# Performance work log

Hardware: AMD Instinct MI355X
Metric: run time of the kernel (lower is better)

## Reference

```python
import jax, jax.numpy as jnp
import numpy as np

K_NEIGHBORS = 32  # n_neighbors, eval mode -> displacement = 0


def setup_inputs() -> dict:
    key = jax.random.key(0)
    ks = jax.random.split(key, 9)
    B, N, F = 1024, 200000, 64
    C, H = 16, 128
    return {
        "x": jax.random.normal(ks[0], (B, F), jnp.float32),
        "X_data": jax.random.normal(ks[1], (N, F), jnp.float32),
        "y": jax.random.uniform(ks[2], (N,), jnp.float32),
        "W_gate": jax.random.normal(ks[3], (F + 1, C), jnp.float32) / np.sqrt(F + 1),
        "b_gate": jax.random.normal(ks[4], (C,), jnp.float32) * 0.01,
        "W1": jax.random.normal(ks[5], (C + F, H), jnp.float32) / np.sqrt(C + F),
        "b1": jax.random.normal(ks[6], (H,), jnp.float32) * 0.01,
        "W_last": jax.random.normal(ks[7], (H, 1), jnp.float32) / np.sqrt(H),
        "b_last": jax.random.normal(ks[8], (1,), jnp.float32) * 0.01,
    }


def reference(x, X_data, y, W_gate, b_gate, W1, b1, W_last, b_last):
    # Euclidean (p=2) cdist via the expanded form: ||a-b||^2 = ||a||^2 + ||b||^2 - 2 a.b
    d2 = (jnp.sum(x * x, axis=1, keepdims=True)
          + jnp.sum(X_data * X_data, axis=1)[None, :]
          - 2.0 * (x @ X_data.T))                      # [B, N]
    dist = jnp.sqrt(jnp.maximum(d2, 0.0))
    # torch.argsort(distances,1)[:, :k] == indices of k smallest distances
    _, idx = jax.lax.top_k(-dist, K_NEIGHBORS)          # [B, K]
    neighbors = X_data[idx]                             # [B, K, F] gather
    neighbors_y = y[idx][..., None]                     # [B, K, 1]
    nf = jnp.concatenate([neighbors, neighbors_y], axis=2)  # [B, K, F+1]
    gated = jnp.tanh(nf @ W_gate + b_gate)              # [B, K, C]
    agg = jnp.sum(gated, axis=1)                        # [B, C]
    o = jnp.concatenate([x, agg], axis=1)               # [B, F+C]
    o = jnp.tanh(o @ W1 + b1)                           # activation_function = tanh
    o = jax.nn.sigmoid(o @ W_last + b_last)             # [B, 1]
    return o
```

## Files before the change

### kernel.cpp

```cpp
#include <hip/hip_runtime.h>
#include <cstdint>

#define FDIM 64
#define KNN 32
#define NBUCKET 256
#define MAXCAP 2048
#define SEG 8
#define OCAP 512
#define BANDQ 96

typedef unsigned int u32;
typedef unsigned long long u64;
typedef __attribute__((ext_vector_type(8))) short bf16x8;
typedef __attribute__((ext_vector_type(4))) float f32x4;

__device__ __forceinline__ void gload_lds16(const void* g, void* l) {
    __builtin_amdgcn_global_load_lds(
        (const __attribute__((address_space(1))) unsigned int*)g,
        (__attribute__((address_space(3))) unsigned int*)l,
        16, 0, 0);
}

__device__ __forceinline__ float load_query(const float* __restrict__ x, int q, float4* xv) {
    const float4* xp = (const float4*)(x + (size_t)q * FDIM);
    float n0 = 0.f, n1 = 0.f, n2 = 0.f, n3 = 0.f;
#pragma unroll
    for (int k = 0; k < 16; ++k) {
        float4 v = xp[k];
        xv[k] = v;
        n0 = fmaf(v.x, v.x, n0); n1 = fmaf(v.y, v.y, n1);
        n2 = fmaf(v.z, v.z, n2); n3 = fmaf(v.w, v.w, n3);
    }
    return (n0 + n1) + (n2 + n3);
}

__device__ __forceinline__ float dot_row(const float4* __restrict__ xv, const float* __restrict__ row) {
    const float4* rv = (const float4*)row;
    float d0 = 0.f, d1 = 0.f, d2 = 0.f, d3 = 0.f;
#pragma unroll
    for (int k = 0; k < 16; ++k) {
        float4 r = rv[k];
        float4 a = xv[k];
        d0 = fmaf(a.x, r.x, d0); d1 = fmaf(a.y, r.y, d1);
        d2 = fmaf(a.z, r.z, d2); d3 = fmaf(a.w, r.w, d3);
    }
    return (d0 + d1) + (d2 + d3);
}

__global__ __launch_bounds__(256) void k_xnorm(const float* __restrict__ X, float* __restrict__ Xn, int N) {
    int i = blockIdx.x * 256 + threadIdx.x;
    if (i >= N) return;
    const float4* r = (const float4*)(X + (size_t)i * FDIM);
    float d0 = 0.f, d1 = 0.f, d2 = 0.f, d3 = 0.f;
#pragma unroll
    for (int k = 0; k < 16; ++k) {
        float4 v = r[k];
        d0 = fmaf(v.x, v.x, d0); d1 = fmaf(v.y, v.y, d1);
        d2 = fmaf(v.z, v.z, d2); d3 = fmaf(v.w, v.w, d3);
    }
    Xn[i] = (d0 + d1) + (d2 + d3);
}

__global__ __launch_bounds__(256) void k_cvtT(const float* __restrict__ src, uint4* __restrict__ dst, int n_u4) {
    int i = blockIdx.x * 256 + threadIdx.x;
    if (i >= n_u4) return;
    int lane = i & 63;
    int kk = (i >> 6) & 1;
    int g = i >> 7;
    int row = g * 16 + (lane & 15);
    int col = kk * 32 + (lane >> 4) * 8;
    const float4* s = (const float4*)(src + (size_t)row * FDIM + col);
    float4 a = s[0], b = s[1];
    ushort o[8];
    const float* f = &a.x;
#pragma unroll
    for (int k = 0; k < 4; ++k) {
        u32 u = __float_as_uint(f[k]);
        o[k] = (ushort)((u + 0x7fffu + ((u >> 16) & 1u)) >> 16);
    }
    const float* gg = &b.x;
#pragma unroll
    for (int k = 0; k < 4; ++k) {
        u32 u = __float_as_uint(gg[k]);
        o[4 + k] = (ushort)((u + 0x7fffu + ((u >> 16) & 1u)) >> 16);
    }
    dst[i] = *(uint4*)o;
}

__global__ __launch_bounds__(256) void k_cvtT_norm(const float* __restrict__ src, uint4* __restrict__ dst,
                                                   float* __restrict__ norms, int n_u4) {
    __shared__ float pn[4][16];
    int t = threadIdx.x;
    int i = blockIdx.x * 256 + t;
    int lane = t & 63;
    int w = t >> 6;
    int kk = (i >> 6) & 1;
    int g = i >> 7;
    int r = lane & 15;
    int row = g * 16 + r;
    int col = kk * 32 + (lane >> 4) * 8;
    const float4* s = (const float4*)(src + (size_t)row * FDIM + col);
    float4 a = s[0], b = s[1];
    float n0 = fmaf(a.x, a.x, a.y * a.y);
    float n1 = fmaf(a.z, a.z, a.w * a.w);
    float n2 = fmaf(b.x, b.x, b.y * b.y);
    float n3 = fmaf(b.z, b.z, b.w * b.w);
    float ss = (n0 + n1) + (n2 + n3);
    ushort o[8];
    const float* f = &a.x;
#pragma unroll
    for (int k = 0; k < 4; ++k) {
        u32 u = __float_as_uint(f[k]);
        o[k] = (ushort)((u + 0x7fffu + ((u >> 16) & 1u)) >> 16);
    }
    const float* gg = &b.x;
#pragma unroll
    for (int k = 0; k < 4; ++k) {
        u32 u = __float_as_uint(gg[k]);
        o[4 + k] = (ushort)((u + 0x7fffu + ((u >> 16) & 1u)) >> 16);
    }
    dst[i] = *(uint4*)o;
    ss += __shfl_xor(ss, 16);
    ss += __shfl_xor(ss, 32);
    if (lane < 16) pn[w][r] = ss;
    __syncthreads();
    if (t < 32) {
        float v = (t < 16) ? (pn[0][t] + pn[1][t]) : (pn[2][t - 16] + pn[3][t - 16]);
        norms[blockIdx.x * 32 + t] = v;
    }
}

__global__ __launch_bounds__(256) void k_hist(const float* __restrict__ x, const float* __restrict__ X,
                                              const float* __restrict__ Xn, u32* __restrict__ hist,
                                              int N, int nsamp, int sj) {
    __shared__ unsigned char h8[NBUCKET * 256];
    int t = threadIdx.x;
    u32* h32 = (u32*)h8;
#pragma unroll
    for (int k = 0; k < 64; ++k) h32[k * 256 + t] = 0;
    __syncthreads();
    int q = blockIdx.x * 256 + t;
    float4 xv[16];
    float xn = load_query(x, q, xv);
    for (int j = 0; j < sj; ++j) {
        int s = blockIdx.y * sj + j;
        int p = s * 16;
        if (s < nsamp && p < N) {
            float dp = dot_row(xv, X + (size_t)p * FDIM);
            float d2 = fmaxf(xn + Xn[p] - 2.f * dp, 0.f);
            int b = min(NBUCKET - 1, (int)d2);
            int idx = b * 256 + t;
            unsigned char v = h8[idx];
            h8[idx] = (v == 255u) ? v : (unsigned char)(v + 1);
        }
    }
    __syncthreads();
#pragma unroll
    for (int w = 0; w < 128; ++w) {
        u32 v0 = h8[(2 * w) * 256 + t];
        u32 v1 = h8[(2 * w + 1) * 256 + t];
        if (v0 | v1) atomicAdd(&hist[(size_t)q * 128 + w], v0 | (v1 << 16));
    }
}

__global__ __launch_bounds__(256) void k_thresh(const u32* __restrict__ hist, float* __restrict__ Tq, int B) {
    int q = blockIdx.x * 256 + threadIdx.x;
    if (q >= B) return;
    const u32* h = hist + (size_t)q * 128;
    int cum = 0;
    float T = (float)NBUCKET;
    for (int w = 0; w < 128; ++w) {
        u32 v = h[w];
        cum += (int)(v & 0xffffu);
        if (cum >= KNN) { T = (float)(2 * w + 1); break; }
        cum += (int)(v >> 16);
        if (cum >= KNN) { T = (float)(2 * w + 2); break; }
    }
    Tq[q] = T + 2.0f;
}

__global__ __launch_bounds__(256, 3) void k_sample_d2(
        const uint4* __restrict__ xT, const uint4* __restrict__ XT,
        const float* __restrict__ qn, const float* __restrict__ Xn,
        unsigned char* __restrict__ d2s, int S) {
    int t = threadIdx.x;
    int w = t >> 6, lane = t & 63;
    int G = lane >> 4, r = lane & 15;
    int qg = blockIdx.x;
    int wq = qg * 128 + w * 32;
    int pb = blockIdx.y * 128;
    int Bq = gridDim.x * 128;

    bf16x8 afr[2][2];
#pragma unroll
    for (int kk = 0; kk < 2; ++kk)
#pragma unroll
        for (int mi = 0; mi < 2; ++mi) {
            uint4 v = xT[(size_t)(((wq >> 4) + mi) * 2 + kk) * 64 + lane];
            afr[kk][mi] = *(bf16x8*)&v;
        }
    float qr[8];
#pragma unroll
    for (int e = 0; e < 8; ++e)
        qr[e] = qn[wq + (e >> 2) * 16 + G * 4 + (e & 3)];

    unsigned char* dtile = d2s + (size_t)blockIdx.y * Bq * 128;

#pragma unroll
    for (int half = 0; half < 2; ++half) {
        int nb = half * 4;
        bf16x8 bfr[4][2];
#pragma unroll
        for (int j = 0; j < 4; ++j) {
            int gp = (pb >> 4) + nb + j;
#pragma unroll
            for (int kk = 0; kk < 2; ++kk) {
                uint4 v = XT[(size_t)(gp * 2 + kk) * 64 + lane];
                bfr[j][kk] = *(bf16x8*)&v;
            }
        }
        float xnv[4];
#pragma unroll
        for (int j = 0; j < 4; ++j) xnv[j] = Xn[pb + (nb + j) * 16 + r];

        f32x4 acc[2][4];
#pragma unroll
        for (int mi = 0; mi < 2; ++mi)
#pragma unroll
            for (int j = 0; j < 4; ++j) acc[mi][j] = (f32x4){0.f, 0.f, 0.f, 0.f};
#pragma unroll
        for (int kk = 0; kk < 2; ++kk)
#pragma unroll
            for (int j = 0; j < 4; ++j) {
                acc[0][j] = __builtin_amdgcn_mfma_f32_16x16x32_bf16(afr[kk][0], bfr[j][kk], acc[0][j], 0, 0, 0);
                acc[1][j] = __builtin_amdgcn_mfma_f32_16x16x32_bf16(afr[kk][1], bfr[j][kk], acc[1][j], 0, 0, 0);
            }
#pragma unroll
        for (int j = 0; j < 4; ++j) {
            int pl = (nb + j) * 16 + r;
            float xnp = xnv[j];
#pragma unroll
            for (int e = 0; e < 8; ++e) {
                float d2a = qr[e] + fmaf(-2.f, acc[e >> 2][j][e & 3], xnp);
                int b = (int)d2a;
                b = b < 0 ? 0 : (b > 255 ? 255 : b);
                int q = wq + (e >> 2) * 16 + G * 4 + (e & 3);
                dtile[(size_t)q * 128 + pl] = (unsigned char)b;
            }
        }
    }
}

__global__ __launch_bounds__(256) void k_thresh2(const unsigned char* __restrict__ d2s,
                                                 float* __restrict__ Tq, int S) {
    __shared__ u32 h[4][NBUCKET];
    int t = threadIdx.x;
    int w = t >> 6;
    int q = blockIdx.x;
    int Bq = gridDim.x;
#pragma unroll
    for (int k = 0; k < 4; ++k) h[k][t] = 0;
    __syncthreads();
    const u32* base32 = (const u32*)d2s;
    int n32 = S >> 2;
    for (int i = t; i < n32; i += 256) {
        int tile = i >> 5, c = i & 31;
        u32 v = base32[((size_t)tile * Bq + q) * 32 + c];
        u32* hw = h[w];
        atomicAdd(&hw[v & 255u], 1u);
        atomicAdd(&hw[(v >> 8) & 255u], 1u);
        atomicAdd(&hw[(v >> 16) & 255u], 1u);
        atomicAdd(&hw[v >> 24], 1u);
    }
    __syncthreads();
    u32 s = h[0][t] + h[1][t] + h[2][t] + h[3][t];
    h[0][t] = s;
    __syncthreads();
    if (t == 0) {
        int cum = 0;
        float T = 256.0f;
        for (int b = 0; b < NBUCKET; ++b) {
            cum += (int)h[0][b];
            if (cum >= KNN) { T = (float)(b + 1); break; }
        }
        Tq[q] = T + 2.0f;
    }
}

__global__ __launch_bounds__(256, 4) void k_mfma_filter(
        const uint4* __restrict__ xT, const uint4* __restrict__ XT,
        const float* __restrict__ qn, const float* __restrict__ Xn,
        const float* __restrict__ Tf,
        u32* __restrict__ cnt_seg, u32* __restrict__ list_seg,
        u32* __restrict__ ocnt, u32* __restrict__ olist,
        int N, int nStripsPad, int strip, int B) {
    __shared__ uint4 sbuf[1024];
    __shared__ u32 ldsCnt[128];

    int t = threadIdx.x;
    int w = t >> 6, lane = t & 63;
    int G = lane >> 4, r = lane & 15;

    int bid = blockIdx.x;
    int qg = (bid >> 3) & 7;
    int sIdx = (bid & 7) | ((bid >> 6) << 3);
    int qbase = qg * 128;
    int wq = qbase + w * 32;

    if (t < 128) ldsCnt[t] = 0;

    bf16x8 afr[2][2];
#pragma unroll
    for (int kk = 0; kk < 2; ++kk)
#pragma unroll
        for (int mi = 0; mi < 2; ++mi) {
            uint4 v = xT[(size_t)(((wq >> 4) + mi) * 2 + kk) * 64 + lane];
            afr[kk][mi] = *(bf16x8*)&v;
        }
    float nT[8], qnr[8];
#pragma unroll
    for (int e = 0; e < 8; ++e) {
        int rl = wq + (e >> 2) * 16 + G * 4 + (e & 3);
        float qv = qn[rl];
        qnr[e] = qv;
        nT[e] = -0.5f * (Tf[rl] - qv);
    }

    u32* segBase = list_seg + ((size_t)qbase * nStripsPad + (size_t)sIdx) * SEG;

    int pb0 = sIdx * strip * 128;
    int ntl = (pb0 < N) ? strip : 0;

    for (int s = 0; s < ntl; ++s) {
        int pb = pb0 + s * 128;
        {
            const char* src = (const char*)XT + (size_t)(pb >> 4) * 2048 + w * 1024 + lane * 16;
            char* dst = (char*)&sbuf[0] + w * 1024;
            gload_lds16(src, dst);
            gload_lds16(src + 4096, dst + 4096);
            gload_lds16(src + 8192, dst + 8192);
            gload_lds16(src + 12288, dst + 12288);
        }
        __syncthreads();
        const uint4* cur = &sbuf[0];

#pragma unroll
        for (int half = 0; half < 2; ++half) {
            int nb = half * 4;
            bf16x8 bfr[4][2];
#pragma unroll
            for (int j = 0; j < 4; ++j) {
#pragma unroll
                for (int kk = 0; kk < 2; ++kk) {
                    uint4 v = cur[((nb + j) * 2 + kk) * 64 + lane];
                    bfr[j][kk] = *(bf16x8*)&v;
                }
            }
            float xnv[4], ai[4];
#pragma unroll
            for (int j = 0; j < 4; ++j) {
                xnv[j] = Xn[pb + (nb + j) * 16 + r];
                ai[j] = -0.5f * xnv[j];
            }

            f32x4 acc[2][4];
#pragma unroll
            for (int mi = 0; mi < 2; ++mi)
#pragma unroll
                for (int j = 0; j < 4; ++j) acc[mi][j] = (f32x4){ai[j], ai[j], ai[j], ai[j]};
#pragma unroll
            for (int kk = 0; kk < 2; ++kk)
#pragma unroll
                for (int j = 0; j < 4; ++j) {
                    acc[0][j] = __builtin_amdgcn_mfma_f32_16x16x32_bf16(afr[kk][0], bfr[j][kk], acc[0][j], 0, 0, 0);
                    acc[1][j] = __builtin_amdgcn_mfma_f32_16x16x32_bf16(afr[kk][1], bfr[j][kk], acc[1][j], 0, 0, 0);
                }
#pragma unroll
            for (int j = 0; j < 4; ++j) {
                int p = pb + (nb + j) * 16 + r;
                bool ce[8];
#pragma unroll
                for (int e = 0; e < 8; ++e)
                    ce[e] = acc[e >> 2][j][e & 3] > nT[e];
                if ((ce[0] | ce[1] | ce[2] | ce[3] | ce[4] | ce[5] | ce[6] | ce[7]) && p < N) {
#pragma unroll
                    for (int e = 0; e < 8; ++e) {
                        if (ce[e]) {
                            float d2a = fmaf(-2.f, acc[e >> 2][j][e & 3], qnr[e]);
                            d2a = d2a < 0.f ? 0.f : d2a;
                            u32 dq = (u32)(d2a * 32.f);
                            if (dq > 16383u) dq = 16383u;
                            u32 key = (dq << 18) | (u32)p;
                            int ql = w * 32 + (e >> 2) * 16 + G * 4 + (e & 3);
                            u32 slot = atomicAdd(&ldsCnt[ql], 1u);
                            if (slot < SEG) {
                                segBase[(size_t)ql * nStripsPad * SEG + slot] = key;
                            } else {
                                u32 gs = atomicAdd(&ocnt[qbase + ql], 1u);
                                if (gs < OCAP) olist[(size_t)(qbase + ql) * OCAP + gs] = key;
                            }
                        }
                    }
                }
            }
        }
        __syncthreads();
    }

    if (ntl == 0) __syncthreads();
    if (t < 128) cnt_seg[(size_t)sIdx * B + qbase + t] = min(ldsCnt[t], (u32)SEG);
}

__global__ __launch_bounds__(256) void k_filter_scalar(const float* __restrict__ x, const float* __restrict__ X,
                                                       const float* __restrict__ Xn, const float* __restrict__ Tq,
                                                       u32* __restrict__ cnt, u32* __restrict__ list,
                                                       int N, int cap) {
    int t = threadIdx.x;
    int q = blockIdx.x * 256 + t;
    float4 xv[16];
    float xn = load_query(x, q, xv);
    float T = Tq[q];
    int base = blockIdx.y * 1024;
    int lim = min(1024, N - base);
    for (int j = 0; j < lim; ++j) {
        int p = base + j;
        float dp = dot_row(xv, X + (size_t)p * FDIM);
        float d2 = fmaxf(xn + Xn[p] - 2.f * dp, 0.f);
        if (d2 < T) {
            u32 slot = atomicAdd(&cnt[q], 1u);
            if (slot < (u32)cap) list[(size_t)q * cap + slot] = (u32)p;
        }
    }
}

__global__ __launch_bounds__(256) void k_final(const float* __restrict__ x, const float* __restrict__ X,
                                               const float* __restrict__ y, const float* __restrict__ Xn,
                                               const float* __restrict__ Wg, const float* __restrict__ bg,
                                               const float* __restrict__ W1, const float* __restrict__ b1,
                                               const float* __restrict__ Wl, const float* __restrict__ bl,
                                               const u32* __restrict__ cnt_seg, const u32* __restrict__ list_seg,
                                               const u32* __restrict__ ocnt, const u32* __restrict__ olist,
                                               const u32* __restrict__ cnt_flat, const u32* __restrict__ list_flat,
                                               float* __restrict__ out, int nStripsPad, int cap_flat, int flat,
                                               int N, int B) {
    __shared__ u64 keys[MAXCAP];
    __shared__ u32 nsh;
    __shared__ u64 wk[4];
    __shared__ int wp[4];
    __shared__ u32 sel[KNN];
    __shared__ float gkc[KNN * 16];
    __shared__ float aggc[16];
    __shared__ float red[128];
    __shared__ u32 hist[2048];
    __shared__ u32 wtot[4];
    __shared__ u32 cutq_sh;
    __shared__ u32 nrs;

    int t = threadIdx.x;
    int w = t >> 6, lane = t & 63;
    int q = blockIdx.x;
    int m;

    if (flat) {
        m = (int)min(cnt_flat[q], (u32)cap_flat);
        const u32* lq = list_flat + (size_t)q * cap_flat;
        for (int i = t; i < m; i += 256) keys[i] = lq[i];
    } else {
        if (t == 0) nsh = 0;
        __syncthreads();
        for (int seg = t; seg < nStripsPad; seg += 256) {
            u32 c = cnt_seg[(size_t)seg * B + q];
            if (c) {
                u32 base = atomicAdd(&nsh, c);
                const u32* sp = list_seg + ((size_t)q * nStripsPad + seg) * SEG;
                for (u32 j = 0; j < c; ++j) {
                    u32 idx = base + j;
                    if (idx < MAXCAP) keys[idx] = sp[j];
                }
            }
        }
        __syncthreads();
        int m0 = (int)min(nsh, (u32)MAXCAP);
        int oc = (int)min(ocnt[q], (u32)OCAP);
        for (int i = t; i < oc; i += 256)
            if (m0 + i < MAXCAP) keys[m0 + i] = olist[(size_t)q * OCAP + i];
        m = min(m0 + oc, MAXCAP);
    }
    __syncthreads();

    if (!flat) {
        for (int i = t; i < 2048; i += 256) hist[i] = 0;
        if (t == 0) cutq_sh = 0xFFFFFFFFu;
        __syncthreads();
        for (int i = t; i < m; i += 256) atomicAdd(&hist[((u32)keys[i]) >> 21], 1u);
        __syncthreads();
        u32 s = 0;
#pragma unroll
        for (int j = 0; j < 8; ++j) s += hist[t * 8 + j];
        u32 run = s;
#pragma unroll
        for (int off = 1; off < 64; off <<= 1) {
            u32 v = __shfl_up(run, off);
            if (lane >= off) run += v;
        }
        if (lane == 63) wtot[w] = run;
        __syncthreads();
        u32 wo = 0;
#pragma unroll
        for (int v = 0; v < 4; ++v) wo += (v < w) ? wtot[v] : 0u;
        u32 inc = wo + run;
        u32 exc = inc - s;
        if (exc < (u32)KNN && inc >= (u32)KNN) {
            u32 cum = exc;
#pragma unroll
            for (int j = 0; j < 8; ++j) {
                cum += hist[t * 8 + j];
                if (cum >= (u32)KNN) { cutq_sh = (u32)(((t * 8 + j + 1) << 3) + BANDQ); break; }
            }
        }
    }
    if (t == 0) nrs = 0;
    __syncthreads();
    u32 cutq = flat ? 0xFFFFFFFFu : cutq_sh;

    u32* cand = hist;
    for (int i = t; i < m; i += 256) {
        u32 k = (u32)keys[i];
        if ((k >> 18) <= cutq) cand[atomicAdd(&nrs, 1u)] = k & 0x3FFFFu;
    }
    __syncthreads();
    int mr = (int)min(nrs, (u32)MAXCAP);

    {
        int ch = lane & 15;
        int rsub = lane >> 4;
        float4 xq4 = ((const float4*)(x + (size_t)q * FDIM))[ch];
        float xs = fmaf(xq4.x, xq4.x, fmaf(xq4.y, xq4.y, fmaf(xq4.z, xq4.z, xq4.w * xq4.w)));
        xs += __shfl_xor(xs, 1);
        xs += __shfl_xor(xs, 2);
        xs += __shfl_xor(xs, 4);
        xs += __shfl_xor(xs, 8);
        float xn = xs;
        for (int base = w * 32; base < mr; base += 128) {
            int ri[8]; u32 pp[8]; bool val[8]; float4 vv[8];
#pragma unroll
            for (int u = 0; u < 8; ++u) {
                ri[u] = base + u * 4 + rsub;
                val[u] = ri[u] < mr;
                pp[u] = val[u] ? cand[ri[u]] : 0u;
            }
#pragma unroll
            for (int u = 0; u < 8; ++u)
                vv[u] = ((const float4*)(X + (size_t)pp[u] * FDIM))[ch];
#pragma unroll
            for (int u = 0; u < 8; ++u) {
                float part = fmaf(xq4.x, vv[u].x, fmaf(xq4.y, vv[u].y, fmaf(xq4.z, vv[u].z, xq4.w * vv[u].w)));
                part += __shfl_xor(part, 1);
                part += __shfl_xor(part, 2);
                part += __shfl_xor(part, 4);
                part += __shfl_xor(part, 8);
                if (val[u] && ch == 0) {
                    float d2 = fmaxf(xn + Xn[pp[u]] - 2.f * part, 0.f);
                    keys[ri[u]] = ((u64)__float_as_uint(d2) << 32) | pp[u];
                }
            }
        }
    }
    __syncthreads();

    if (mr <= 512) {
        if (w == 0) {
            u64 rk[8];
#pragma unroll
            for (int i = 0; i < 8; ++i) {
                int idx = lane + (i << 6);
                rk[i] = (idx < mr) ? keys[idx] : ~0ull;
            }
            for (int r = 0; r < KNN; ++r) {
                u64 bk = ~0ull;
                int bs = 0;
#pragma unroll
                for (int i = 0; i < 8; ++i)
                    if (rk[i] < bk) { bk = rk[i]; bs = i; }
                int bo = lane;
#pragma unroll
                for (int off = 1; off < 64; off <<= 1) {
                    u64 ok = __shfl_xor(bk, off);
                    int oo = __shfl_xor(bo, off);
                    if (ok < bk) { bk = ok; bo = oo; }
                }
                if (lane == bo) rk[bs] = ~0ull;
                if (lane == 0) sel[r] = (u32)bk;
            }
        }
        __syncthreads();
    } else {
        for (int r = 0; r < KNN; ++r) {
            u64 bk = ~0ull;
            int bp = -1;
            for (int i = t; i < mr; i += 256) {
                u64 k = keys[i];
                if (k < bk) { bk = k; bp = i; }
            }
#pragma unroll
            for (int off = 32; off > 0; off >>= 1) {
                u64 ok = __shfl_down(bk, off);
                int op = __shfl_down(bp, off);
                if (ok < bk) { bk = ok; bp = op; }
            }
            if (lane == 0) { wk[w] = bk; wp[w] = bp; }
            __syncthreads();
            if (t == 0) {
                u64 fb = wk[0];
                int fp = wp[0];
                for (int v = 1; v < 4; ++v)
                    if (wk[v] < fb) { fb = wk[v]; fp = wp[v]; }
                sel[r] = (u32)(fb & 0xffffffffu);
                if (fp >= 0) keys[fp] = ~0ull;
            }
            __syncthreads();
        }
    }

    int c = t & 15, kk = t >> 4;
#pragma unroll
    for (int rep = 0; rep < 2; ++rep) {
        int k = kk + 16 * rep;
        int nb = min((int)sel[k], N - 1);
        const float* Xr = X + (size_t)nb * FDIM;
        float acc = bg[c];
#pragma unroll
        for (int f = 0; f < FDIM; ++f) acc = fmaf(Xr[f], Wg[f * 16 + c], acc);
        acc = fmaf(y[nb], Wg[FDIM * 16 + c], acc);
        gkc[k * 16 + c] = tanhf(acc);
    }
    __syncthreads();
    if (t < 16) {
        float s = 0.f;
#pragma unroll
        for (int k = 0; k < KNN; ++k) s += gkc[k * 16 + t];
        aggc[t] = s;
    }
    __syncthreads();
    if (t < 128) {
        const float* xq = x + (size_t)q * FDIM;
        float acc = b1[t];
#pragma unroll
        for (int f = 0; f < FDIM; ++f) acc = fmaf(xq[f], W1[f * 128 + t], acc);
#pragma unroll
        for (int cc2 = 0; cc2 < 16; ++cc2) acc = fmaf(aggc[cc2], W1[(FDIM + cc2) * 128 + t], acc);
        red[t] = tanhf(acc) * Wl[t];
    }
    __syncthreads();
    for (int off = 64; off > 0; off >>= 1) {
        if (t < off) red[t] += red[t + off];
        __syncthreads();
    }
    if (t == 0) out[q] = 1.f / (1.f + expf(-(red[0] + bl[0])));
}

extern "C" void kernel_launch(void* const* d_in, const int* in_sizes, int n_in,
                              void* d_out, int out_size, void* d_ws, size_t ws_size,
                              hipStream_t stream) {
    const float* x  = (const float*)d_in[0];
    const float* X  = (const float*)d_in[1];
    const float* y  = (const float*)d_in[2];
    const float* Wg = (const float*)d_in[3];
    const float* bg = (const float*)d_in[4];
    const float* W1 = (const float*)d_in[5];
    const float* b1 = (const float*)d_in[6];
    const float* Wl = (const float*)d_in[7];
    const float* bl = (const float*)d_in[8];
    float* out = (float*)d_out;

    int B = in_sizes[0] / FDIM;
    int N = in_sizes[1] / FDIM;

    const int strip = 4;
    int nTiles = (N + 127) / 128;
    int nStrips = (nTiles + strip - 1) / strip;
    nStrips = (nStrips + 7) & ~7;
    int nStripsPad = nStrips;
    int Npad = nStrips * strip * 128;

    char* w = (char*)d_ws;
    size_t off = 0;
    auto alloc = [&](size_t bytes) { void* p = w + off; off += (bytes + 255) & ~(size_t)255; return p; };
    float* Xn  = (float*)alloc((size_t)Npad * 4);
    float* qn  = (float*)alloc((size_t)B * 4);
    u32* hist  = (u32*)alloc((size_t)B * 512);
    float* Tq  = (float*)alloc((size_t)B * 4);
    u32* cnt   = (u32*)alloc((size_t)B * 4);

    size_t xTB = (size_t)B * 128;
    size_t XTB = (size_t)(Npad / 16) * 2048;
    size_t segCntB = (size_t)B * nStripsPad * 4;
    size_t segListB = (size_t)B * nStripsPad * SEG * 4;
    size_t ocntB = (size_t)B * 4;
    size_t olistB = (size_t)B * OCAP * 4;
    size_t rem = (ws_size > off) ? ws_size - off : 0;
    bool mfma_path = rem >= xTB + XTB + segCntB + segListB + ocntB + olistB + 4096;

    uint4* xT = nullptr; uint4* XT = nullptr;
    u32 *cnt_seg = nullptr, *list_seg = nullptr, *ocnt = nullptr, *olist = nullptr;
    u32* list_flat = nullptr; unsigned char* d2s = nullptr;
    int cap_flat = 64, Stiles = 0;
    if (mfma_path) {
        xT = (uint4*)alloc(xTB);
        XT = (uint4*)alloc(XTB);
        cnt_seg  = (u32*)alloc(segCntB);
        list_seg = (u32*)alloc(segListB);
        ocnt     = (u32*)alloc(ocntB);
        olist    = (u32*)alloc(olistB);
        rem = (ws_size > off) ? ws_size - off : 0;
        size_t st = rem / ((size_t)B * 128);
        Stiles = st > 100 ? 100 : (int)st;
        int maxFull = N / 128;
        if (Stiles > maxFull) Stiles = maxFull;
        if (Stiles >= 96) d2s = (unsigned char*)alloc((size_t)Stiles * 128 * B);
        else Stiles = 0;
    } else {
        size_t c = rem / ((size_t)B * 4);
        cap_flat = c > MAXCAP ? MAXCAP : (int)c;
        if (cap_flat < 64) cap_flat = 64;
        list_flat = (u32*)alloc((size_t)B * cap_flat * 4);
    }

    if (mfma_path) {
        hipMemsetAsync(ocnt, 0, ocntB, stream);
        hipMemsetAsync(Xn + N, 0, (size_t)(Npad - N) * 4, stream);
        size_t realXT = (size_t)(N / 16) * 2048;
        hipMemsetAsync((char*)XT + realXT, 0, XTB - realXT, stream);

        int nxu4 = B * 8, nXu4 = N * 8;
        if ((nxu4 & 255) == 0) {
            k_cvtT_norm<<<dim3(nxu4 / 256), 256, 0, stream>>>(x, xT, qn, nxu4);
        } else {
            k_xnorm<<<dim3((B + 255) / 256), 256, 0, stream>>>(x, qn, B);
            k_cvtT<<<dim3((nxu4 + 255) / 256), 256, 0, stream>>>(x, xT, nxu4);
        }
        if ((nXu4 & 255) == 0) {
            k_cvtT_norm<<<dim3(nXu4 / 256), 256, 0, stream>>>(X, XT, Xn, nXu4);
        } else {
            k_xnorm<<<dim3((N + 255) / 256), 256, 0, stream>>>(X, Xn, N);
            k_cvtT<<<dim3((nXu4 + 255) / 256), 256, 0, stream>>>(X, XT, nXu4);
        }

        if (Stiles > 0) {
            int S = Stiles * 128;
            k_sample_d2<<<dim3(8, Stiles), 256, 0, stream>>>(xT, XT, qn, Xn, d2s, S);
            k_thresh2<<<dim3(B), 256, 0, stream>>>(d2s, Tq, S);
        } else {
            hipMemsetAsync(hist, 0, (size_t)B * 512, stream);
            int nsamp = (N + 15) / 16;
            int chunks = 128;
            int sj = (nsamp + chunks - 1) / chunks;
            k_hist<<<dim3(B / 256, chunks), 256, 0, stream>>>(x, X, Xn, hist, N, nsamp, sj);
            k_thresh<<<dim3((B + 255) / 256), 256, 0, stream>>>(hist, Tq, B);
        }

        k_mfma_filter<<<dim3(8 * nStrips), 256, 0, stream>>>(
            xT, XT, qn, Xn, Tq, cnt_seg, list_seg, ocnt, olist, N, nStripsPad, strip, B);

        k_final<<<dim3(B), 256, 0, stream>>>(x, X, y, Xn, Wg, bg, W1, b1, Wl, bl,
                                             cnt_seg, list_seg, ocnt, olist,
                                             nullptr, nullptr, out, nStripsPad, 0, 0, N, B);
    } else {
        k_xnorm<<<dim3((N + 255) / 256), 256, 0, stream>>>(X, Xn, N);
        k_xnorm<<<dim3((B + 255) / 256), 256, 0, stream>>>(x, qn, B);
        hipMemsetAsync(cnt, 0, (size_t)B * 4, stream);
        hipMemsetAsync(hist, 0, (size_t)B * 512, stream);
        int nsamp = (N + 15) / 16;
        int chunks = 128;
        int sj = (nsamp + chunks - 1) / chunks;
        k_hist<<<dim3(B / 256, chunks), 256, 0, stream>>>(x, X, Xn, hist, N, nsamp, sj);
        k_thresh<<<dim3((B + 255) / 256), 256, 0, stream>>>(hist, Tq, B);
        k_filter_scalar<<<dim3(B / 256, (N + 1023) / 1024), 256, 0, stream>>>(
            x, X, Xn, Tq, cnt, list_flat, N, cap_flat);
        k_final<<<dim3(B), 256, 0, stream>>>(x, X, y, Xn, Wg, bg, W1, b1, Wl, bl,
                                             nullptr, nullptr, nullptr, nullptr,
                                             cnt, list_flat, out, nStripsPad, cap_flat, 1, N, B);
    }
}
```

Measured before the change: 244.2 us.

## Fuse query/data bf16 conversion kernels, fold memsets, and halve threshold histogram bins

Merges the two transpose/convert-and-norm launches into one kernel that zero-pads the out-of-range rows itself. This removes three memsets, and the ocnt reset now happens inside the threshold kernel. It also doubles the resolution of the sampled-distance histogram buckets (0.5 width), which tightens the per-query threshold so fewer candidates pass the filter. The finer bins clip at 128 instead of 256, which risks saturating the threshold for far queries. The old path is kept for shapes that do not divide evenly.

```diff
diff --git a/kernel.cpp b/kernel.cpp
--- a/kernel.cpp
+++ b/kernel.cpp
@@ -87,20 +87,32 @@
     dst[i] = *(uint4*)o;
 }
 
-__global__ __launch_bounds__(256) void k_cvtT_norm(const float* __restrict__ src, uint4* __restrict__ dst,
-                                                   float* __restrict__ norms, int n_u4) {
+__global__ __launch_bounds__(256) void k_cvtT_norm2(
+        const float* __restrict__ xsrc, const float* __restrict__ Xsrc,
+        uint4* __restrict__ xdst, uint4* __restrict__ Xdst,
+        float* __restrict__ qn, float* __restrict__ Xn,
+        int xBlocks, int xRows, int XRowsReal) {
     __shared__ float pn[4][16];
     int t = threadIdx.x;
-    int i = blockIdx.x * 256 + t;
     int lane = t & 63;
     int w = t >> 6;
+    int r = lane & 15;
+    const float* src; uint4* dst; float* norms; int realRows; int lb;
+    if ((int)blockIdx.x < xBlocks) {
+        lb = blockIdx.x; src = xsrc; dst = xdst; norms = qn; realRows = xRows;
+    } else {
+        lb = blockIdx.x - xBlocks; src = Xsrc; dst = Xdst; norms = Xn; realRows = XRowsReal;
+    }
+    int i = lb * 256 + t;
     int kk = (i >> 6) & 1;
     int g = i >> 7;
-    int r = lane & 15;
     int row = g * 16 + r;
     int col = kk * 32 + (lane >> 4) * 8;
-    const float4* s = (const float4*)(src + (size_t)row * FDIM + col);
-    float4 a = s[0], b = s[1];
+    float4 a = {0.f, 0.f, 0.f, 0.f}, b = {0.f, 0.f, 0.f, 0.f};
+    if (row < realRows) {
+        const float4* s = (const float4*)(src + (size_t)row * FDIM + col);
+        a = s[0]; b = s[1];
+    }
     float n0 = fmaf(a.x, a.x, a.y * a.y);
     float n1 = fmaf(a.z, a.z, a.w * a.w);
     float n2 = fmaf(b.x, b.x, b.y * b.y);
@@ -126,7 +138,7 @@
     __syncthreads();
     if (t < 32) {
         float v = (t < 16) ? (pn[0][t] + pn[1][t]) : (pn[2][t - 16] + pn[3][t - 16]);
-        norms[blockIdx.x * 32 + t] = v;
+        norms[lb * 32 + t] = v;
     }
 }
 
@@ -242,7 +254,7 @@
 #pragma unroll
             for (int e = 0; e < 8; ++e) {
                 float d2a = qr[e] + fmaf(-2.f, acc[e >> 2][j][e & 3], xnp);
-                int b = (int)d2a;
+                int b = (int)(d2a * 2.0f);
                 b = b < 0 ? 0 : (b > 255 ? 255 : b);
                 int q = wq + (e >> 2) * 16 + G * 4 + (e & 3);
                 dtile[(size_t)q * 128 + pl] = (unsigned char)b;
@@ -252,12 +264,13 @@
 }
 
 __global__ __launch_bounds__(256) void k_thresh2(const unsigned char* __restrict__ d2s,
-                                                 float* __restrict__ Tq, int S) {
+                                                 float* __restrict__ Tq, u32* __restrict__ ocnt, int S) {
     __shared__ u32 h[4][NBUCKET];
     int t = threadIdx.x;
     int w = t >> 6;
     int q = blockIdx.x;
     int Bq = gridDim.x;
+    if (t == 0) ocnt[q] = 0;
 #pragma unroll
     for (int k = 0; k < 4; ++k) h[k][t] = 0;
     __syncthreads();
@@ -278,10 +291,10 @@
     __syncthreads();
     if (t == 0) {
         int cum = 0;
-        float T = 256.0f;
+        float T = 128.0f;
         for (int b = 0; b < NBUCKET; ++b) {
             cum += (int)h[0][b];
-            if (cum >= KNN) { T = (float)(b + 1); break; }
+            if (cum >= KNN) { T = 0.5f * (float)(b + 1); break; }
         }
         Tq[q] = T + 2.0f;
     }
@@ -726,38 +739,40 @@
         list_flat = (u32*)alloc((size_t)B * cap_flat * 4);
     }
 
-    if (mfma_path) {
+    if (mfma_path && Stiles > 0 && (B % 32) == 0 && (N % 32) == 0) {
+        int xBlocks = B / 32;
+        int XPadBlocks = Npad / 32;
+        k_cvtT_norm2<<<dim3(xBlocks + XPadBlocks), 256, 0, stream>>>(
+            x, X, xT, XT, qn, Xn, xBlocks, B, N);
+
+        int S = Stiles * 128;
+        k_sample_d2<<<dim3(8, Stiles), 256, 0, stream>>>(xT, XT, qn, Xn, d2s, S);
+        k_thresh2<<<dim3(B), 256, 0, stream>>>(d2s, Tq, ocnt, S);
+
+        k_mfma_filter<<<dim3(8 * nStrips), 256, 0, stream>>>(
+            xT, XT, qn, Xn, Tq, cnt_seg, list_seg, ocnt, olist, N, nStripsPad, strip, B);
+
+        k_final<<<dim3(B), 256, 0, stream>>>(x, X, y, Xn, Wg, bg, W1, b1, Wl, bl,
+                                             cnt_seg, list_seg, ocnt, olist,
+                                             nullptr, nullptr, out, nStripsPad, 0, 0, N, B);
+    } else if (mfma_path) {
         hipMemsetAsync(ocnt, 0, ocntB, stream);
         hipMemsetAsync(Xn + N, 0, (size_t)(Npad - N) * 4, stream);
         size_t realXT = (size_t)(N / 16) * 2048;
         hipMemsetAsync((char*)XT + realXT, 0, XTB - realXT, stream);
 
         int nxu4 = B * 8, nXu4 = N * 8;
-        if ((nxu4 & 255) == 0) {
-            k_cvtT_norm<<<dim3(nxu4 / 256), 256, 0, stream>>>(x, xT, qn, nxu4);
-        } else {
-            k_xnorm<<<dim3((B + 255) / 256), 256, 0, stream>>>(x, qn, B);
-            k_cvtT<<<dim3((nxu4 + 255) / 256), 256, 0, stream>>>(x, xT, nxu4);
-        }
-        if ((nXu4 & 255) == 0) {
-            k_cvtT_norm<<<dim3(nXu4 / 256), 256, 0, stream>>>(X, XT, Xn, nXu4);
-        } else {
-            k_xnorm<<<dim3((N + 255) / 256), 256, 0, stream>>>(X, Xn, N);
-            k_cvtT<<<dim3((nXu4 + 255) / 256), 256, 0, stream>>>(X, XT, nXu4);
-        }
-
-        if (Stiles > 0) {
-            int S = Stiles * 128;
-            k_sample_d2<<<dim3(8, Stiles), 256, 0, stream>>>(xT, XT, qn, Xn, d2s, S);
-            k_thresh2<<<dim3(B), 256, 0, stream>>>(d2s, Tq, S);
-        } else {
-            hipMemsetAsync(hist, 0, (size_t)B * 512, stream);
-            int nsamp = (N + 15) / 16;
-            int chunks = 128;
-            int sj = (nsamp + chunks - 1) / chunks;
-            k_hist<<<dim3(B / 256, chunks), 256, 0, stream>>>(x, X, Xn, hist, N, nsamp, sj);
-            k_thresh<<<dim3((B + 255) / 256), 256, 0, stream>>>(hist, Tq, B);
-        }
+        k_xnorm<<<dim3((B + 255) / 256), 256, 0, stream>>>(x, qn, B);
+        k_cvtT<<<dim3((nxu4 + 255) / 256), 256, 0, stream>>>(x, xT, nxu4);
+        k_xnorm<<<dim3((N + 255) / 256), 256, 0, stream>>>(X, Xn, N);
+        k_cvtT<<<dim3((nXu4 + 255) / 256), 256, 0, stream>>>(X, XT, nXu4);
+
+        hipMemsetAsync(hist, 0, (size_t)B * 512, stream);
+        int nsamp = (N + 15) / 16;
+        int chunks = 128;
+        int sj = (nsamp + chunks - 1) / chunks;
+        k_hist<<<dim3(B / 256, chunks), 256, 0, stream>>>(x, X, Xn, hist, N, nsamp, sj);
+        k_thresh<<<dim3((B + 255) / 256), 256, 0, stream>>>(hist, Tq, B);
 
         k_mfma_filter<<<dim3(8 * nStrips), 256, 0, stream>>>(
             xT, XT, qn, Xn, Tq, cnt_seg, list_seg, ocnt, olist, N, nStripsPad, strip, B);
```

New measurement: 269.5 us. 10.4% more time.
